# Kernel optimization log

Measured on AMD Instinct MI355X. Metric: run time of the kernel, lower is better.

The kernel has to match this reference:

```python
import jax, jax.numpy as jnp
import numpy as np
import math

H = 16          # num heads
D = 64          # head dim
MAX_POS = 512   # max_position_embeddings


def setup_inputs() -> dict:
    key = jax.random.key(0)
    ks = jax.random.split(key, 8)
    B, S, E = 8, 512, 1024
    scale = 1.0 / math.sqrt(E)
    return {
        "hidden_states": jax.random.normal(ks[0], (B, S, E), jnp.float32),
        "attention_mask": jnp.zeros((B, 1, 1, S), jnp.float32),
        "Wq": jax.random.normal(ks[1], (E, E), jnp.float32) * scale,
        "bq": jnp.zeros((E,), jnp.float32),
        "Wk": jax.random.normal(ks[2], (E, E), jnp.float32) * scale,
        "bk": jnp.zeros((E,), jnp.float32),
        "Wv": jax.random.normal(ks[3], (E, E), jnp.float32) * scale,
        "bv": jnp.zeros((E,), jnp.float32),
        "dist_emb": jax.random.normal(ks[4], (2 * MAX_POS - 1, D), jnp.float32) * 0.02,
    }


def reference(hidden_states, attention_mask, Wq, bq, Wk, bk, Wv, bv, dist_emb):
    B, S, E = hidden_states.shape

    def heads(x):  # [B,S,E] -> [B,H,S,D]
        return x.reshape(B, S, H, D).transpose(0, 2, 1, 3)

    q = heads(hidden_states @ Wq + bq)
    k = heads(hidden_states @ Wk + bk)
    v = heads(hidden_states @ Wv + bv)

    # raw scores [B,H,S,S]
    scores = jnp.einsum('bhld,bhrd->bhlr', q, k)

    # relative position embedding lookup: distance[l,r] = l - r
    pos = jnp.arange(S)
    distance = pos[:, None] - pos[None, :]               # [S,S]
    pe = dist_emb[distance + MAX_POS - 1]                # [S,S,D]
    scores = scores + jnp.einsum('bhld,lrd->bhlr', q, pe)
    scores = scores + jnp.einsum('bhrd,lrd->bhlr', k, pe)

    scores = scores / math.sqrt(D) + attention_mask
    probs = jax.nn.softmax(scores, axis=-1)

    ctx = jnp.einsum('bhlr,bhrd->bhld', probs, v)        # [B,H,S,D]
    ctx = ctx.transpose(0, 2, 1, 3).reshape(B, S, H * D)
    return ctx
```

## Files before the change

kernel.cpp:

```cpp
#include <hip/hip_runtime.h>

#define BATCH 8
#define SEQ   512
#define EMB   1024
#define NH    16
#define HD    64

typedef __bf16 bf16x8 __attribute__((ext_vector_type(8)));
typedef float  f32x4  __attribute__((ext_vector_type(4)));

__device__ __forceinline__ unsigned short f2bf(float f){
  return __builtin_bit_cast(unsigned short, (__bf16)f);
}
__device__ __forceinline__ float bf2f(unsigned short s){
  union { unsigned u; float f; } v; v.u = ((unsigned)s) << 16;
  return v.f;
}

__device__ __forceinline__ float dpp_max16(float x){
  int t;
  t = __builtin_amdgcn_update_dpp(0, __builtin_bit_cast(int, x), 0xB1, 0xF, 0xF, true);
  x = fmaxf(x, __builtin_bit_cast(float, t));
  t = __builtin_amdgcn_update_dpp(0, __builtin_bit_cast(int, x), 0x4E, 0xF, 0xF, true);
  x = fmaxf(x, __builtin_bit_cast(float, t));
  t = __builtin_amdgcn_update_dpp(0, __builtin_bit_cast(int, x), 0x141, 0xF, 0xF, true);
  x = fmaxf(x, __builtin_bit_cast(float, t));
  t = __builtin_amdgcn_update_dpp(0, __builtin_bit_cast(int, x), 0x140, 0xF, 0xF, true);
  x = fmaxf(x, __builtin_bit_cast(float, t));
  return x;
}
__device__ __forceinline__ float dpp_sum16(float x){
  int t;
  t = __builtin_amdgcn_update_dpp(0, __builtin_bit_cast(int, x), 0xB1, 0xF, 0xF, true);
  x += __builtin_bit_cast(float, t);
  t = __builtin_amdgcn_update_dpp(0, __builtin_bit_cast(int, x), 0x4E, 0xF, 0xF, true);
  x += __builtin_bit_cast(float, t);
  t = __builtin_amdgcn_update_dpp(0, __builtin_bit_cast(int, x), 0x141, 0xF, 0xF, true);
  x += __builtin_bit_cast(float, t);
  t = __builtin_amdgcn_update_dpp(0, __builtin_bit_cast(int, x), 0x140, 0xF, 0xF, true);
  x += __builtin_bit_cast(float, t);
  return x;
}

__device__ __forceinline__ int swzc(int row, int chunk){
  return row * 128 + (((chunk ^ (row & 7)) & 7) << 4);
}
__device__ __forceinline__ int swz2(int row, int col){
  return row * 128 + ((((col >> 3) ^ (row & 7)) & 7) << 4) + ((col & 7) << 1);
}

__device__ __forceinline__ void gload16(const unsigned short* g, unsigned char* lds){
  __builtin_amdgcn_global_load_lds((const __attribute__((address_space(1))) unsigned int*)g,
                                   (__attribute__((address_space(3))) unsigned int*)lds,
                                   16, 0, 0);
}

__device__ __forceinline__ void bar_lds(){
  asm volatile("s_waitcnt lgkmcnt(0)" ::: "memory");
  __builtin_amdgcn_s_barrier();
}

__global__ void k_pre(const float* __restrict__ hid, unsigned short* __restrict__ hidb,
                      const float* __restrict__ dist, unsigned short* __restrict__ distb,
                      const float* __restrict__ Wq, const float* __restrict__ Wk,
                      const float* __restrict__ Wv, unsigned short* __restrict__ wqt,
                      unsigned short* __restrict__ wkt, unsigned short* __restrict__ wvt){
  int bid = blockIdx.x;
  int t = threadIdx.x;
  if (bid < 4096){
    int i = (bid * 256 + t) * 4;
    float4 v = *(const float4*)(hid + i);
    ushort4 o; o.x = f2bf(v.x); o.y = f2bf(v.y); o.z = f2bf(v.z); o.w = f2bf(v.w);
    *(ushort4*)(hidb + i) = o;
  } else if (bid < 4352){
    int i = (bid - 4096) * 256 + t;
    distb[i] = (i < 1023 * 64) ? f2bf(dist[i]) : (unsigned short)0;
  } else {
    int wt = bid - 4352;
    int z = wt >> 10, rem = wt & 1023;
    const float* W = (z == 0) ? Wq : (z == 1) ? Wk : Wv;
    unsigned short* WT = (z == 0) ? wqt : (z == 1) ? wkt : wvt;
    __shared__ float tl[32][33];
    int n0 = (rem & 31) * 32, k0 = (rem >> 5) * 32;
    int tx = t & 31, ty = t >> 5;
#pragma unroll
    for (int i = 0; i < 4; i++)
      tl[ty + 8*i][tx] = W[(k0 + ty + 8*i) * EMB + n0 + tx];
    __syncthreads();
#pragma unroll
    for (int i = 0; i < 4; i++)
      WT[(n0 + ty + 8*i) * EMB + k0 + tx] = f2bf(tl[tx][ty + 8*i]);
  }
}

__global__ __launch_bounds__(256, 3) void k_gemm3(const unsigned short* __restrict__ A,
                                                  const unsigned short* __restrict__ wqt,
                                                  const unsigned short* __restrict__ wkt,
                                                  const unsigned short* __restrict__ wvt,
                                                  const float* __restrict__ bq,
                                                  const float* __restrict__ bk,
                                                  const float* __restrict__ bv,
                                                  unsigned short* __restrict__ qb,
                                                  unsigned short* __restrict__ kb,
                                                  unsigned short* __restrict__ vtb){
  int z = blockIdx.z;
  const unsigned short* BT = (z == 0) ? wqt : (z == 1) ? wkt : wvt;
  const float* bias = (z == 0) ? bq : (z == 1) ? bk : bv;
  unsigned short* out = (z == 0) ? qb : (z == 1) ? kb : vtb;
  int mode = (z == 2);

  __shared__ __align__(16) unsigned char sA[128 * 128];
  __shared__ __align__(16) unsigned char sB[128 * 128];
  int m0 = blockIdx.y * 128, n0 = blockIdx.x * 128;
  int t = threadIdx.x, w = t >> 6, lane = t & 63, g = lane >> 4, lr = lane & 15;
  int rowbase = (w >> 1) * 64, colbase = (w & 1) * 64;
  int lrow = lane >> 3, lc = lane & 7;
  f32x4 acc[4][4] = {};
  for (int k0 = 0; k0 < EMB; k0 += 64){
    __syncthreads();
#pragma unroll
    for (int i = 0; i < 4; i++){
      int row = (w + 4*i) * 8 + lrow;
      int cg  = lc ^ (row & 7);
      gload16(A  + (m0 + row) * EMB + k0 + cg*8, sA + (w + 4*i) * 1024);
      gload16(BT + (n0 + row) * EMB + k0 + cg*8, sB + (w + 4*i) * 1024);
    }
    __syncthreads();
#pragma unroll
    for (int kk = 0; kk < 2; kk++){
      bf16x8 af[4], bfv[4];
#pragma unroll
      for (int i = 0; i < 4; i++) af[i]  = *(const bf16x8*)(sA + swzc(rowbase + 16*i + lr, kk*4 + g));
#pragma unroll
      for (int j = 0; j < 4; j++) bfv[j] = *(const bf16x8*)(sB + swzc(colbase + 16*j + lr, kk*4 + g));
#pragma unroll
      for (int i = 0; i < 4; i++)
#pragma unroll
        for (int j = 0; j < 4; j++)
          acc[i][j] = __builtin_amdgcn_mfma_f32_16x16x32_bf16(af[i], bfv[j], acc[i][j], 0, 0, 0);
    }
  }
#pragma unroll
  for (int i = 0; i < 4; i++)
#pragma unroll
    for (int j = 0; j < 4; j++)
#pragma unroll
      for (int r = 0; r < 4; r++){
        int m = m0 + rowbase + 16*i + 4*g + r;
        int n = n0 + colbase + 16*j + lr;
        float val = acc[i][j][r] + bias[n];
        int b = m >> 9, s = m & 511, h = n >> 6, d = n & 63;
        int idx = (mode == 0) ? (((b*NH + h)*SEQ + s)*HD + d)
                              : (((b*NH + h)*HD + d)*SEQ + s);
        out[idx] = f2bf(val);
      }
}

__global__ __launch_bounds__(512, 2) void k_attn(const unsigned short* __restrict__ qb,
                                                 const unsigned short* __restrict__ kb,
                                                 const unsigned short* __restrict__ vtb,
                                                 const unsigned short* __restrict__ distb,
                                                 const float* __restrict__ mask,
                                                 float* __restrict__ out){
  __shared__ __align__(16) unsigned char sK[64 * 128];
  __shared__ __align__(16) unsigned char sV[64 * 128];
  __shared__ __align__(16) unsigned char sSA[8][2624];
  __shared__ __align__(16) unsigned char sSB[8][2560];

  const float SCL  = 0.125f * 1.4426950408889634f;
  const float L2E  = 1.4426950408889634f;

  int bid = blockIdx.x;
  int wgid = (bid & 7) * 64 + (bid >> 3);
  int lt = wgid & 3, h = (wgid >> 2) & 15, b = wgid >> 6;
  int L0 = lt * 128;
  int bh = b * NH + h;
  int t = threadIdx.x, w = t >> 6, lane = t & 63, g = lane >> 4, lr = lane & 15;
  int lbase = 16 * w;
  unsigned char* mySA = sSA[w];
  unsigned char* mySB = sSB[w];
  unsigned char* myP  = mySA;
  const float* maskp = mask + b * SEQ;

  const unsigned short* qrow = qb + (bh * SEQ + L0 + lbase + lr) * HD + 8 * g;
  bf16x8 aq0 = *(const bf16x8*)qrow;
  bf16x8 aq1 = *(const bf16x8*)(qrow + 32);

  bf16x8 pe[5][2];
#define LOAD_PE(JB) do {                                                     \
    const unsigned short* _pb = distb + ((JB) + 16*w + lr) * HD + 8*g;       \
    _Pragma("unroll")                                                        \
    for (int _j = 0; _j < 5; _j++){                                          \
      pe[_j][0] = *(const bf16x8*)(_pb + _j*16*HD);                          \
      pe[_j][1] = *(const bf16x8*)(_pb + _j*16*HD + 32); }                   \
  } while(0)

  int lrow = lane >> 3, lc = lane & 7;
  int row0 = w * 8 + lrow;
  int cg0  = lc ^ (row0 & 7);
  const unsigned short* kbase = kb  + bh * SEQ * HD;
  const unsigned short* vbase = vtb + bh * HD * SEQ;

  uint4 kst0 = *(const uint4*)(kbase + row0 * HD  + cg0 * 8);
  uint4 vst0 = *(const uint4*)(vbase + row0 * SEQ + cg0 * 8);
  LOAD_PE(L0 + 448);

  f32x4 o[4] = {};
  float mrun[4], srun[4];
#pragma unroll
  for (int r = 0; r < 4; r++){ mrun[r] = -1e30f; srun[r] = 0.f; }

  for (int rt = 0; rt < 8; rt++){
    int R0 = rt * 64;

    bar_lds();

    *(uint4*)(sK + w * 1024 + lane * 16) = kst0;
    *(uint4*)(sV + w * 1024 + lane * 16) = vst0;

    if (rt < 7){
      kst0 = *(const uint4*)(kbase + (R0 + 64) * HD + row0 * HD  + cg0 * 8);
      vst0 = *(const uint4*)(vbase + (R0 + 64)      + row0 * SEQ + cg0 * 8);
    }

    float mreg[4];
#pragma unroll
    for (int f = 0; f < 4; f++) mreg[f] = maskp[R0 + 16*f + lr];

    bar_lds();

    __builtin_amdgcn_s_setprio(1);
    f32x4 sc[4];
#pragma unroll
    for (int f = 0; f < 4; f++){
      bf16x8 k0 = *(const bf16x8*)(sK + swzc(16*f + lr, g));
      bf16x8 k1 = *(const bf16x8*)(sK + swzc(16*f + lr, 4 + g));
      f32x4 a = {};
      a = __builtin_amdgcn_mfma_f32_16x16x32_bf16(aq0, k0, a, 0, 0, 0);
      a = __builtin_amdgcn_mfma_f32_16x16x32_bf16(aq1, k1, a, 0, 0, 0);
      sc[f] = a;
      f32x4 b0 = {}, b1 = {};
      b0 = __builtin_amdgcn_mfma_f32_16x16x32_bf16(k0, pe[3 - f][0], b0, 0, 0, 0);
      b0 = __builtin_amdgcn_mfma_f32_16x16x32_bf16(k1, pe[3 - f][1], b0, 0, 0, 0);
      b1 = __builtin_amdgcn_mfma_f32_16x16x32_bf16(k0, pe[4 - f][0], b1, 0, 0, 0);
      b1 = __builtin_amdgcn_mfma_f32_16x16x32_bf16(k1, pe[4 - f][1], b1, 0, 0, 0);
#pragma unroll
      for (int reg = 0; reg < 4; reg++){
        int ss = 4*g + reg + lr;
        float v = (ss >= 15) ? b0[reg] : b1[reg];
        int row = 16*f + 4*g + reg;
        int col = (ss + 1) & 15;
        *(__bf16*)(mySB + row*40 + col*2) = (__bf16)v;
      }
    }

#pragma unroll
    for (int jt2 = 0; jt2 < 5; jt2++){
      f32x4 a = {};
      a = __builtin_amdgcn_mfma_f32_16x16x32_bf16(aq0, pe[jt2][0], a, 0, 0, 0);
      a = __builtin_amdgcn_mfma_f32_16x16x32_bf16(aq1, pe[jt2][1], a, 0, 0, 0);
#pragma unroll
      for (int reg = 0; reg < 4; reg++){
        int rloc = 63 + 4*g + reg - lr - 16*jt2;
        int addr = ((unsigned)rloc < 64u) ? (rloc*40 + (4*g + reg)*2) : 2560;
        *(__bf16*)(mySA + addr) = (__bf16)a[reg];
      }
    }
    __builtin_amdgcn_s_setprio(0);

    if (rt < 7) LOAD_PE(L0 + 448 - 64*(rt + 1));

#pragma unroll
    for (int f = 0; f < 4; f++){
      ushort4 sa = *(const ushort4*)(mySA + (16*f + lr)*40 + 8*g);
      ushort4 sb = *(const ushort4*)(mySB + (16*f + lr)*40 + 8*g);
      float madd = mreg[f] * L2E;
      sc[f][0] = (sc[f][0] + bf2f(sa.x) + bf2f(sb.x)) * SCL + madd;
      sc[f][1] = (sc[f][1] + bf2f(sa.y) + bf2f(sb.y)) * SCL + madd;
      sc[f][2] = (sc[f][2] + bf2f(sa.z) + bf2f(sb.z)) * SCL + madd;
      sc[f][3] = (sc[f][3] + bf2f(sa.w) + bf2f(sb.w)) * SCL + madd;
    }

    float tm[4];
    bool sml = true;
#pragma unroll
    for (int r = 0; r < 4; r++){
      float t0 = fmaxf(fmaxf(sc[0][r], sc[1][r]), fmaxf(sc[2][r], sc[3][r]));
      tm[r] = dpp_max16(t0);
      sml = sml && (tm[r] - mrun[r] <= 8.0f);
    }
    if (__all(sml)){
#pragma unroll
      for (int r = 0; r < 4; r++){
        float ps = 0.f;
#pragma unroll
        for (int f = 0; f < 4; f++){ float p = exp2f(sc[f][r] - mrun[r]); sc[f][r] = p; ps += p; }
        ps = dpp_sum16(ps);
        srun[r] += ps;
      }
    } else {
#pragma unroll
      for (int r = 0; r < 4; r++){
        float mnew = fmaxf(mrun[r], tm[r]);
        float fr = exp2f(mrun[r] - mnew);
        float ps = 0.f;
#pragma unroll
        for (int f = 0; f < 4; f++){ float p = exp2f(sc[f][r] - mnew); sc[f][r] = p; ps += p; }
        ps = dpp_sum16(ps);
        srun[r] = srun[r] * fr + ps;
        mrun[r] = mnew;
#pragma unroll
        for (int df = 0; df < 4; df++) o[df][r] *= fr;
      }
    }

#pragma unroll
    for (int f = 0; f < 4; f++)
#pragma unroll
      for (int r = 0; r < 4; r++)
        *(__bf16*)(myP + swz2(4*g + r, 16*f + lr)) = (__bf16)sc[f][r];

    __builtin_amdgcn_s_setprio(1);
#pragma unroll
    for (int kk = 0; kk < 2; kk++){
      bf16x8 pf = *(const bf16x8*)(myP + swzc(lr, kk*4 + g));
#pragma unroll
      for (int df = 0; df < 4; df++){
        bf16x8 vf = *(const bf16x8*)(sV + swzc(16*df + lr, kk*4 + g));
        o[df] = __builtin_amdgcn_mfma_f32_16x16x32_bf16(pf, vf, o[df], 0, 0, 0);
      }
    }
    __builtin_amdgcn_s_setprio(0);
  }

#pragma unroll
  for (int r = 0; r < 4; r++){
    float inv = 1.0f / srun[r];
#pragma unroll
    for (int df = 0; df < 4; df++){
      int l = L0 + lbase + 4*g + r;
      out[(b * SEQ + l) * EMB + h * HD + 16*df + lr] = o[df][r] * inv;
    }
  }
#undef LOAD_PE
}

extern "C" void kernel_launch(void* const* d_in, const int* in_sizes, int n_in,
                              void* d_out, int out_size, void* d_ws, size_t ws_size,
                              hipStream_t stream) {
  (void)in_sizes; (void)n_in; (void)out_size; (void)ws_size;
  const float* hid  = (const float*)d_in[0];
  const float* mask = (const float*)d_in[1];
  const float* Wq   = (const float*)d_in[2];
  const float* bq   = (const float*)d_in[3];
  const float* Wk   = (const float*)d_in[4];
  const float* bk   = (const float*)d_in[5];
  const float* Wv   = (const float*)d_in[6];
  const float* bv   = (const float*)d_in[7];
  const float* dist = (const float*)d_in[8];
  float* out = (float*)d_out;

  unsigned char* ws = (unsigned char*)d_ws;
  unsigned short* hidb  = (unsigned short*)ws;
  unsigned short* wqt   = hidb + 4096 * 1024;
  unsigned short* wkt   = wqt  + 1024 * 1024;
  unsigned short* wvt   = wkt  + 1024 * 1024;
  unsigned short* distb = wvt  + 1024 * 1024;
  unsigned short* qb    = distb + 1024 * 64;
  unsigned short* kb    = qb + BATCH * NH * SEQ * HD;
  unsigned short* vtb   = kb + BATCH * NH * SEQ * HD;

  k_pre<<<7424, 256, 0, stream>>>(hid, hidb, dist, distb, Wq, Wk, Wv, wqt, wkt, wvt);
  k_gemm3<<<dim3(8, 32, 3), 256, 0, stream>>>(hidb, wqt, wkt, wvt, bq, bk, bv, qb, kb, vtb);
  k_attn<<<512, 512, 0, stream>>>(qb, kb, vtb, distb, mask, out);
}
```

Measured before the change: 104.1 us.

## Double-buffer K/V tiles in LDS and always rescale in online softmax

K and V tiles now live in two LDS buffers. The next tile is stored into the alternate buffer while the current one is consumed, and the global prefetch runs two tiles ahead. This removes one of the two workgroup barriers in each iteration. The lazy-rescale branch in the online softmax, which skipped rescaling unless the max grew by more than a threshold, is replaced with an unconditional max update and accumulator rescale. That drops the wave vote and the divergent path but adds an exp and multiplies on every iteration. LDS use rises by 16 KB per block, which may press on occupancy at two blocks per CU.

```diff
diff --git a/kernel.cpp b/kernel.cpp
--- a/kernel.cpp
+++ b/kernel.cpp
@@ -162,8 +162,8 @@
                                                  const unsigned short* __restrict__ distb,
                                                  const float* __restrict__ mask,
                                                  float* __restrict__ out){
-  __shared__ __align__(16) unsigned char sK[64 * 128];
-  __shared__ __align__(16) unsigned char sV[64 * 128];
+  __shared__ __align__(16) unsigned char sK[2][64 * 128];
+  __shared__ __align__(16) unsigned char sV[2][64 * 128];
   __shared__ __align__(16) unsigned char sSA[8][2624];
   __shared__ __align__(16) unsigned char sSB[8][2560];
 
@@ -203,6 +203,10 @@
 
   uint4 kst0 = *(const uint4*)(kbase + row0 * HD  + cg0 * 8);
   uint4 vst0 = *(const uint4*)(vbase + row0 * SEQ + cg0 * 8);
+  *(uint4*)(sK[0] + w * 1024 + lane * 16) = kst0;
+  *(uint4*)(sV[0] + w * 1024 + lane * 16) = vst0;
+  kst0 = *(const uint4*)(kbase + 64 * HD + row0 * HD  + cg0 * 8);
+  vst0 = *(const uint4*)(vbase + 64      + row0 * SEQ + cg0 * 8);
   LOAD_PE(L0 + 448);
 
   f32x4 o[4] = {};
@@ -212,29 +216,29 @@
 
   for (int rt = 0; rt < 8; rt++){
     int R0 = rt * 64;
+    int cur = rt & 1, nxt = cur ^ 1;
 
     bar_lds();
 
-    *(uint4*)(sK + w * 1024 + lane * 16) = kst0;
-    *(uint4*)(sV + w * 1024 + lane * 16) = vst0;
-
     if (rt < 7){
-      kst0 = *(const uint4*)(kbase + (R0 + 64) * HD + row0 * HD  + cg0 * 8);
-      vst0 = *(const uint4*)(vbase + (R0 + 64)      + row0 * SEQ + cg0 * 8);
+      *(uint4*)(sK[nxt] + w * 1024 + lane * 16) = kst0;
+      *(uint4*)(sV[nxt] + w * 1024 + lane * 16) = vst0;
+    }
+    if (rt < 6){
+      kst0 = *(const uint4*)(kbase + (R0 + 128) * HD + row0 * HD  + cg0 * 8);
+      vst0 = *(const uint4*)(vbase + (R0 + 128)      + row0 * SEQ + cg0 * 8);
     }
 
     float mreg[4];
 #pragma unroll
     for (int f = 0; f < 4; f++) mreg[f] = maskp[R0 + 16*f + lr];
-
-    bar_lds();
 
     __builtin_amdgcn_s_setprio(1);
     f32x4 sc[4];
 #pragma unroll
     for (int f = 0; f < 4; f++){
-      bf16x8 k0 = *(const bf16x8*)(sK + swzc(16*f + lr, g));
-      bf16x8 k1 = *(const bf16x8*)(sK + swzc(16*f + lr, 4 + g));
+      bf16x8 k0 = *(const bf16x8*)(sK[cur] + swzc(16*f + lr, g));
+      bf16x8 k1 = *(const bf16x8*)(sK[cur] + swzc(16*f + lr, 4 + g));
       f32x4 a = {};
       a = __builtin_amdgcn_mfma_f32_16x16x32_bf16(aq0, k0, a, 0, 0, 0);
       a = __builtin_amdgcn_mfma_f32_16x16x32_bf16(aq1, k1, a, 0, 0, 0);
@@ -281,38 +285,25 @@
       sc[f][3] = (sc[f][3] + bf2f(sa.w) + bf2f(sb.w)) * SCL + madd;
     }
 
-    float tm[4];
-    bool sml = true;
+    float fac[4];
 #pragma unroll
     for (int r = 0; r < 4; r++){
-      float t0 = fmaxf(fmaxf(sc[0][r], sc[1][r]), fmaxf(sc[2][r], sc[3][r]));
-      tm[r] = dpp_max16(t0);
-      sml = sml && (tm[r] - mrun[r] <= 8.0f);
-    }
-    if (__all(sml)){
-#pragma unroll
-      for (int r = 0; r < 4; r++){
-        float ps = 0.f;
-#pragma unroll
-        for (int f = 0; f < 4; f++){ float p = exp2f(sc[f][r] - mrun[r]); sc[f][r] = p; ps += p; }
-        ps = dpp_sum16(ps);
-        srun[r] += ps;
-      }
-    } else {
-#pragma unroll
-      for (int r = 0; r < 4; r++){
-        float mnew = fmaxf(mrun[r], tm[r]);
-        float fr = exp2f(mrun[r] - mnew);
-        float ps = 0.f;
-#pragma unroll
-        for (int f = 0; f < 4; f++){ float p = exp2f(sc[f][r] - mnew); sc[f][r] = p; ps += p; }
-        ps = dpp_sum16(ps);
-        srun[r] = srun[r] * fr + ps;
-        mrun[r] = mnew;
-#pragma unroll
-        for (int df = 0; df < 4; df++) o[df][r] *= fr;
-      }
-    }
+      float tm = fmaxf(fmaxf(sc[0][r], sc[1][r]), fmaxf(sc[2][r], sc[3][r]));
+      tm = dpp_max16(tm);
+      float mnew = fmaxf(mrun[r], tm);
+      float fr = exp2f(mrun[r] - mnew);
+      float ps = 0.f;
+#pragma unroll
+      for (int f = 0; f < 4; f++){ float p = exp2f(sc[f][r] - mnew); sc[f][r] = p; ps += p; }
+      ps = dpp_sum16(ps);
+      srun[r] = srun[r] * fr + ps;
+      mrun[r] = mnew;
+      fac[r]  = fr;
+    }
+#pragma unroll
+    for (int df = 0; df < 4; df++)
+#pragma unroll
+      for (int r = 0; r < 4; r++) o[df][r] *= fac[r];
 
 #pragma unroll
     for (int f = 0; f < 4; f++)
@@ -326,7 +317,7 @@
       bf16x8 pf = *(const bf16x8*)(myP + swzc(lr, kk*4 + g));
 #pragma unroll
       for (int df = 0; df < 4; df++){
-        bf16x8 vf = *(const bf16x8*)(sV + swzc(16*df + lr, kk*4 + g));
+        bf16x8 vf = *(const bf16x8*)(sV[cur] + swzc(16*df + lr, kk*4 + g));
         o[df] = __builtin_amdgcn_mfma_f32_16x16x32_bf16(pf, vf, o[df], 0, 0, 0);
       }
     }
```

Measured after the change: 105.0 us. No clear change (+0.9%).
